# Kernel optimization log

Hardware: AMD Instinct MI355X
Metric: run time of the kernel (lower is better)

Reference implementation:

```python
import jax, jax.numpy as jnp
import numpy as np

N_NODES = 50000
N_EDGES = 640000
D = 128
BN_EPS = 1e-5
NEG_SLOPE = 0.2  # PyG GATv2Conv default negative_slope


def setup_inputs() -> dict:
    key = jax.random.key(0)
    ks = jax.random.split(key, 8)
    s = 1.0 / np.sqrt(D)
    x = jax.random.normal(ks[0], (N_NODES, D), dtype=jnp.float32)
    edge_index = jax.random.randint(ks[1], (2, N_EDGES), 0, N_NODES, dtype=jnp.int32)
    edge_attr = jax.random.uniform(ks[2], (N_EDGES, 1), dtype=jnp.float32)
    Wl = jax.random.normal(ks[3], (D, D), dtype=jnp.float32) * s
    Wr = jax.random.normal(ks[4], (D, D), dtype=jnp.float32) * s
    We = jax.random.normal(ks[5], (1, D), dtype=jnp.float32) * s
    att = jax.random.normal(ks[6], (D,), dtype=jnp.float32) * s
    return {
        "x": x, "edge_index": edge_index, "edge_attr": edge_attr,
        "Wl": Wl, "bl": jnp.zeros((D,), jnp.float32),
        "Wr": Wr, "br": jnp.zeros((D,), jnp.float32),
        "We": We, "att": att,
        "bias_out": jnp.zeros((D,), jnp.float32),
        "bn_gamma": jnp.ones((D,), jnp.float32),
        "bn_beta": jnp.zeros((D,), jnp.float32),
    }


def _gatv2(x, edge_index, edge_attr, Wl, bl, Wr, br, We, att, bias_out):
    # GATv2Conv, heads=1, concat=True, dropout treated as eval (p=0)
    src, dst = edge_index[0], edge_index[1]
    xl = x @ Wl + bl                      # source-side transform [N, D]
    xr = x @ Wr + br                      # target-side transform [N, D]
    e = edge_attr @ We                    # edge embedding       [E, D]
    m = xl[src] + xr[dst] + e             # gather + fuse        [E, D]
    m = jax.nn.leaky_relu(m, NEG_SLOPE)
    logits = m @ att                      # per-edge score [E]
    n = x.shape[0]
    # segment softmax over destination node neighborhoods
    mx = jax.ops.segment_max(logits, dst, num_segments=n)
    ex = jnp.exp(logits - mx[dst])
    den = jax.ops.segment_sum(ex, dst, num_segments=n)
    alpha = ex / (den[dst] + 1e-16)
    out = jax.ops.segment_sum(xl[src] * alpha[:, None], dst, num_segments=n)
    return out + bias_out


def reference(x, edge_index, edge_attr, Wl, bl, Wr, br, We, att, bias_out,
              bn_gamma, bn_beta):
    h = x + _gatv2(x, edge_index, edge_attr, Wl, bl, Wr, br, We, att, bias_out)
    h = jax.nn.gelu(h, approximate=False)  # torch nn.GELU default (erf)
    # BatchNorm over node dim, training-style batch stats (biased var)
    mean = jnp.mean(h, axis=0)
    var = jnp.mean((h - mean) ** 2, axis=0)
    h = (h - mean) * jax.lax.rsqrt(var + BN_EPS) * bn_gamma + bn_beta
    return h
```

## Files before the change

kernel.cpp:

```cpp
#include <hip/hip_runtime.h>
#include <math.h>

#define D 128
#define STATS_BLOCKS 512
#define SCAN_CHUNK 256

typedef __attribute__((ext_vector_type(8))) short short8;
typedef __attribute__((ext_vector_type(4))) float f32x4;

__device__ __forceinline__ unsigned short f2bf(float f) {
    unsigned u = __float_as_uint(f);
    unsigned r = (u + 0x7fff + ((u >> 16) & 1)) >> 16;
    return (unsigned short)r;
}

__global__ __launch_bounds__(256) void pack_w_k(const float* __restrict__ Wl,
    const float* __restrict__ Wr, unsigned short* __restrict__ wpack)
{
    const int lane = threadIdx.x & 63;
    const int wv = threadIdx.x >> 6;
    const int slot = blockIdx.x * 4 + wv;
    const int ct = slot >> 2;
    const int kt = slot & 3;
    const float* W = (ct < 8) ? Wl : Wr;
    const int cb = (ct & 7) * 16 + (lane & 15);
    const int kb = kt * 32 + (lane >> 4) * 8;
    unsigned short v[8];
#pragma unroll
    for (int i = 0; i < 8; i++) v[i] = f2bf(W[(size_t)(kb + i) * D + cb]);
    *(uint4*)(wpack + ((size_t)slot << 9) + lane * 8) = *(uint4*)v;
}

__global__ __launch_bounds__(256) void gemm_mfma_k(const float* __restrict__ x,
    const unsigned short* __restrict__ wpack, const float* __restrict__ bl,
    const float* __restrict__ br, unsigned* __restrict__ xlb,
    float* __restrict__ xr, int n)
{
    const int lane = threadIdx.x & 63;
    const int wv = threadIdx.x >> 6;
    const int rt = blockIdx.x * 4 + wv;
    if (rt * 16 >= n) return;
    const int r0 = rt * 16;
    const int ra = r0 + (lane & 15);
    const int r = ra < n ? ra : n - 1;
    const int ko = (lane >> 4) * 8;

    short8 a[4];
#pragma unroll
    for (int kt = 0; kt < 4; kt++) {
        const float* px = x + (size_t)r * D + kt * 32 + ko;
        float4 lo = *(const float4*)px;
        float4 hi = *(const float4*)(px + 4);
        short8 t;
        t[0] = (short)f2bf(lo.x); t[1] = (short)f2bf(lo.y);
        t[2] = (short)f2bf(lo.z); t[3] = (short)f2bf(lo.w);
        t[4] = (short)f2bf(hi.x); t[5] = (short)f2bf(hi.y);
        t[6] = (short)f2bf(hi.z); t[7] = (short)f2bf(hi.w);
        a[kt] = t;
    }

    f32x4 acc[16];
#pragma unroll
    for (int i = 0; i < 16; i++) acc[i] = (f32x4){0.f, 0.f, 0.f, 0.f};

#pragma unroll
    for (int kt = 0; kt < 4; kt++) {
#pragma unroll
        for (int ct = 0; ct < 16; ct++) {
            short8 b = *(const short8*)(wpack + (((size_t)(ct * 4 + kt)) << 9) + lane * 8);
            acc[ct] = __builtin_amdgcn_mfma_f32_16x16x32_bf16(a[kt], b, acc[ct], 0, 0, 0);
        }
    }

    const int colb = lane & 15;
    const int rbase = r0 + (lane >> 4) * 4;
#pragma unroll
    for (int ct = 8; ct < 16; ct++) {
        const int c = (ct - 8) * 16 + colb;
        const float bb = br[c];
#pragma unroll
        for (int reg = 0; reg < 4; reg++) {
            const int row = rbase + reg;
            if (row < n) xr[(size_t)row * D + c] = acc[ct][reg] + bb;
        }
    }
#pragma unroll
    for (int ct = 0; ct < 8; ct++) {
        const int c = ct * 16 + colb;
        const float bb = bl[c];
#pragma unroll
        for (int reg = 0; reg < 4; reg++) {
            unsigned mybf = f2bf(acc[ct][reg] + bb);
            unsigned other = (unsigned)__shfl_xor((int)mybf, 1);
            if ((lane & 1) == 0) {
                const int row = rbase + reg;
                if (row < n) xlb[(size_t)row * 64 + (c >> 1)] = mybf | (other << 16);
            }
        }
    }
}

__global__ __launch_bounds__(256) void hist_k(const int* __restrict__ ei,
    int* __restrict__ deg, int E)
{
    int e = blockIdx.x * blockDim.x + threadIdx.x;
    if (e < E) atomicAdd(&deg[ei[E + e]], 1);
}

__global__ __launch_bounds__(256) void scan_sum_k(const int* __restrict__ deg,
    int* __restrict__ bsum, int n)
{
    const int t = threadIdx.x;
    const int i = blockIdx.x * SCAN_CHUNK + t;
    int s = (i < n) ? deg[i] : 0;
#pragma unroll
    for (int off = 32; off > 0; off >>= 1) s += __shfl_xor(s, off);
    __shared__ int ws_[4];
    const int lane = t & 63, w = t >> 6;
    if (lane == 0) ws_[w] = s;
    __syncthreads();
    if (t == 0) bsum[blockIdx.x] = ws_[0] + ws_[1] + ws_[2] + ws_[3];
}

__global__ __launch_bounds__(256) void scan_off_k(const int* __restrict__ bsum,
    int* __restrict__ boff, int* __restrict__ rowptr, int nb, int n)
{
    const int t = threadIdx.x;
    int v = (t < nb) ? bsum[t] : 0;
    const int lane = t & 63, w = t >> 6;
    int inc = v;
#pragma unroll
    for (int off = 1; off < 64; off <<= 1) {
        int u = __shfl_up(inc, off);
        if (lane >= off) inc += u;
    }
    __shared__ int wsum[4], wpre[4];
    if (lane == 63) wsum[w] = inc;
    __syncthreads();
    if (t == 0) {
        int r = 0;
#pragma unroll
        for (int j = 0; j < 4; j++) { wpre[j] = r; r += wsum[j]; }
        rowptr[n] = r;
    }
    __syncthreads();
    if (t < nb) boff[t] = inc - v + wpre[w];
}

__global__ __launch_bounds__(256) void scan_fin_k(int* __restrict__ deg,
    const int* __restrict__ boff, int* __restrict__ rowptr, int n)
{
    const int t = threadIdx.x;
    const int i = blockIdx.x * SCAN_CHUNK + t;
    int v = (i < n) ? deg[i] : 0;
    const int lane = t & 63, w = t >> 6;
    int inc = v;
#pragma unroll
    for (int off = 1; off < 64; off <<= 1) {
        int u = __shfl_up(inc, off);
        if (lane >= off) inc += u;
    }
    __shared__ int wsum[4], wpre[4];
    if (lane == 63) wsum[w] = inc;
    __syncthreads();
    if (t == 0) {
        int r = 0;
#pragma unroll
        for (int j = 0; j < 4; j++) { wpre[j] = r; r += wsum[j]; }
    }
    __syncthreads();
    if (i < n) {
        int ex = inc - v + wpre[w] + boff[blockIdx.x];
        rowptr[i] = ex;
        deg[i] = ex;
    }
}

__global__ __launch_bounds__(256) void scatter_k(const int* __restrict__ ei,
    const float* __restrict__ ea, int* __restrict__ cursor,
    uint2* __restrict__ edges, int E)
{
    int e = blockIdx.x * blockDim.x + threadIdx.x;
    if (e >= E) return;
    int dst = ei[E + e];
    int pos = atomicAdd(&cursor[dst], 1);
    edges[pos] = make_uint2((unsigned)ei[e], __float_as_uint(ea[e]));
}

__global__ __launch_bounds__(256) void agg_k(const unsigned* __restrict__ xlb,
    const float* __restrict__ xr, const int* __restrict__ rowptr,
    const uint2* __restrict__ edges, const float* __restrict__ We,
    const float* __restrict__ att, float* __restrict__ out, int n)
{
    const int wave = threadIdx.x >> 6;
    const int lane = threadIdx.x & 63;
    const int g = lane >> 4;
    const int li = lane & 15;
    const int v = blockIdx.x * 4 + wave;
    if (v >= n) return;
    const int beg = rowptr[v];
    const int end = rowptr[v + 1];

    float xrv[8], wev[8], atv[8];
    {
        const int f0 = li * 8;
        float4 a0 = *(const float4*)(xr + (size_t)v * D + f0);
        float4 a1 = *(const float4*)(xr + (size_t)v * D + f0 + 4);
        xrv[0]=a0.x; xrv[1]=a0.y; xrv[2]=a0.z; xrv[3]=a0.w;
        xrv[4]=a1.x; xrv[5]=a1.y; xrv[6]=a1.z; xrv[7]=a1.w;
        float4 w0 = *(const float4*)(We + f0);
        float4 w1 = *(const float4*)(We + f0 + 4);
        wev[0]=w0.x; wev[1]=w0.y; wev[2]=w0.z; wev[3]=w0.w;
        wev[4]=w1.x; wev[5]=w1.y; wev[6]=w1.z; wev[7]=w1.w;
        float4 t0 = *(const float4*)(att + f0);
        float4 t1 = *(const float4*)(att + f0 + 4);
        atv[0]=t0.x; atv[1]=t0.y; atv[2]=t0.z; atv[3]=t0.w;
        atv[4]=t1.x; atv[5]=t1.y; atv[6]=t1.z; atv[7]=t1.w;
    }

    float m = -1e30f, s = 0.f;
    float acc[8];
#pragma unroll
    for (int k = 0; k < 8; k++) acc[k] = 0.f;

    int j = beg + g;
    uint2 e2 = make_uint2(0u, 0u);
    uint4 xb4 = make_uint4(0u, 0u, 0u, 0u);
    if (j < end) {
        e2 = edges[j];
        xb4 = *(const uint4*)(xlb + (size_t)e2.x * 64 + li * 4);
    }
    while (j < end) {
        const int jn = j + 4;
        const int jc = jn < end ? jn : end - 1;
        uint2 e2n = edges[jc];
        uint4 xbn = *(const uint4*)(xlb + (size_t)e2n.x * 64 + li * 4);

        const float eav = __uint_as_float(e2.y);
        float xv[8];
        xv[0] = __uint_as_float(xb4.x << 16); xv[1] = __uint_as_float(xb4.x & 0xffff0000u);
        xv[2] = __uint_as_float(xb4.y << 16); xv[3] = __uint_as_float(xb4.y & 0xffff0000u);
        xv[4] = __uint_as_float(xb4.z << 16); xv[5] = __uint_as_float(xb4.z & 0xffff0000u);
        xv[6] = __uint_as_float(xb4.w << 16); xv[7] = __uint_as_float(xb4.w & 0xffff0000u);

        float p = 0.f;
#pragma unroll
        for (int k = 0; k < 8; k++) {
            float t = fmaf(eav, wev[k], xrv[k]) + xv[k];
            t = fmaxf(t, 0.2f * t);
            p = fmaf(t, atv[k], p);
        }
#pragma unroll
        for (int off = 8; off >= 1; off >>= 1) p += __shfl_xor(p, off);

        const float pm = fmaxf(m, p);
        const float sc = __expf(m - pm);
        const float w  = __expf(p - pm);
        s = s * sc + w;
#pragma unroll
        for (int k = 0; k < 8; k++) acc[k] = fmaf(acc[k], sc, w * xv[k]);
        m = pm;

        e2 = e2n; xb4 = xbn; j = jn;
    }

#pragma unroll
    for (int off = 16; off <= 32; off <<= 1) {
        const float mo = __shfl_xor(m, off);
        const float so = __shfl_xor(s, off);
        const float pm = fmaxf(m, mo);
        const float sa = __expf(m - pm);
        const float sb = __expf(mo - pm);
        s = s * sa + so * sb;
#pragma unroll
        for (int k = 0; k < 8; k++)
            acc[k] = acc[k] * sa + __shfl_xor(acc[k], off) * sb;
        m = pm;
    }

    if (g == 0) {
        const float inv = 1.f / (s + 1e-16f);
        const int f0 = li * 8;
        float4 o0 = make_float4(acc[0]*inv, acc[1]*inv, acc[2]*inv, acc[3]*inv);
        float4 o1 = make_float4(acc[4]*inv, acc[5]*inv, acc[6]*inv, acc[7]*inv);
        *(float4*)(out + (size_t)v * D + f0) = o0;
        *(float4*)(out + (size_t)v * D + f0 + 4) = o1;
    }
}

__global__ __launch_bounds__(256) void gelu_stats_k(const float* __restrict__ x,
    const float* __restrict__ bias, float* __restrict__ h,
    float* __restrict__ partials, int total4)
{
    const int t = threadIdx.x;
    const int c0 = (t & 31) * 4;
    const float4 bv = *(const float4*)&bias[c0];
    float sum[4] = {0.f, 0.f, 0.f, 0.f}, sq[4] = {0.f, 0.f, 0.f, 0.f};
    const int stride = gridDim.x * blockDim.x;
    for (int i4 = blockIdx.x * blockDim.x + t; i4 < total4; i4 += stride) {
        float4 g4 = ((const float4*)h)[i4];
        float4 xv = ((const float4*)x)[i4];
        float hv[4] = {xv.x + g4.x + bv.x, xv.y + g4.y + bv.y,
                       xv.z + g4.z + bv.z, xv.w + g4.w + bv.w};
        float res[4];
#pragma unroll
        for (int j = 0; j < 4; j++) {
            float ge = 0.5f * hv[j] * (1.f + erff(hv[j] * 0.70710678118654752f));
            res[j] = ge;
            sum[j] += ge;
            sq[j] += ge * ge;
        }
        ((float4*)h)[i4] = make_float4(res[0], res[1], res[2], res[3]);
    }
    __shared__ float red[8][128];
    const int slot = t >> 5;
#pragma unroll
    for (int j = 0; j < 4; j++) red[slot][c0 + j] = sum[j];
    __syncthreads();
    if (t < 128) {
        float tot = 0.f;
#pragma unroll
        for (int s2 = 0; s2 < 8; s2++) tot += red[s2][t];
        partials[(size_t)t * STATS_BLOCKS + blockIdx.x] = tot;
    }
    __syncthreads();
#pragma unroll
    for (int j = 0; j < 4; j++) red[slot][c0 + j] = sq[j];
    __syncthreads();
    if (t < 128) {
        float tot = 0.f;
#pragma unroll
        for (int s2 = 0; s2 < 8; s2++) tot += red[s2][t];
        partials[(size_t)(128 + t) * STATS_BLOCKS + blockIdx.x] = tot;
    }
}

__global__ __launch_bounds__(256) void bn_reduce_params_k(const float* __restrict__ partials,
    const float* __restrict__ gamma, const float* __restrict__ beta,
    float* __restrict__ ab, float n)
{
    const int c = blockIdx.x;
    const int t = threadIdx.x;
    float s = 0.f, q = 0.f;
    for (int b = t; b < STATS_BLOCKS; b += 256) {
        s += partials[(size_t)c * STATS_BLOCKS + b];
        q += partials[(size_t)(128 + c) * STATS_BLOCKS + b];
    }
#pragma unroll
    for (int off = 32; off > 0; off >>= 1) {
        s += __shfl_xor(s, off);
        q += __shfl_xor(q, off);
    }
    __shared__ float ss[4], qq[4];
    const int lane = t & 63, w = t >> 6;
    if (lane == 0) { ss[w] = s; qq[w] = q; }
    __syncthreads();
    if (t == 0) {
        float S = ss[0] + ss[1] + ss[2] + ss[3];
        float Q = qq[0] + qq[1] + qq[2] + qq[3];
        float mean = S / n;
        float var = Q / n - mean * mean;
        float a = rsqrtf(var + 1e-5f) * gamma[c];
        ab[c] = a;
        ab[c + 128] = beta[c] - mean * a;
    }
}

__global__ __launch_bounds__(256) void bn_apply_k(float* __restrict__ h,
    const float* __restrict__ ab, int total4)
{
    int i4 = blockIdx.x * blockDim.x + threadIdx.x;
    if (i4 >= total4) return;
    int cg = i4 & 31;
    float4 v = ((const float4*)h)[i4];
    float4 a = ((const float4*)ab)[cg];
    float4 b = ((const float4*)(ab + 128))[cg];
    ((float4*)h)[i4] = make_float4(v.x * a.x + b.x, v.y * a.y + b.y,
                                   v.z * a.z + b.z, v.w * a.w + b.w);
}

extern "C" void kernel_launch(void* const* d_in, const int* in_sizes, int n_in,
                              void* d_out, int out_size, void* d_ws, size_t ws_size,
                              hipStream_t stream)
{
    const float* x    = (const float*)d_in[0];
    const int*   ei   = (const int*)d_in[1];
    const float* ea   = (const float*)d_in[2];
    const float* Wl   = (const float*)d_in[3];
    const float* bl   = (const float*)d_in[4];
    const float* Wr   = (const float*)d_in[5];
    const float* br   = (const float*)d_in[6];
    const float* We   = (const float*)d_in[7];
    const float* att  = (const float*)d_in[8];
    const float* bias = (const float*)d_in[9];
    const float* gamma= (const float*)d_in[10];
    const float* beta = (const float*)d_in[11];
    float* out = (float*)d_out;

    const int n = in_sizes[0] / D;
    const int E = in_sizes[1] / 2;
    const int nb = (n + SCAN_CHUNK - 1) / SCAN_CHUNK;

    char* ws = (char*)d_ws;
    unsigned short* wpack = (unsigned short*)ws;
    unsigned* xlb = (unsigned*)(ws + 65536);
    float* xr = (float*)(xlb + (size_t)n * 64);
    int* deg = (int*)(xr + (size_t)n * D);
    int* rowptr = deg + n;
    uintptr_t ep = ((uintptr_t)(rowptr + n + 1) + 7) & ~(uintptr_t)7;
    uint2* edges = (uint2*)ep;
    float* partials = (float*)(edges + E);
    int* bsum = (int*)(partials + 256 * STATS_BLOCKS);
    int* boff = bsum + nb;
    float* ab = (float*)(boff + nb);

    hipMemsetAsync(deg, 0, (size_t)n * 4, stream);

    pack_w_k<<<16, 256, 0, stream>>>(Wl, Wr, wpack);
    const int nrt = (n + 15) / 16;
    gemm_mfma_k<<<(nrt + 3) / 4, 256, 0, stream>>>(x, wpack, bl, br, xlb, xr, n);
    hist_k<<<(E + 255) / 256, 256, 0, stream>>>(ei, deg, E);
    scan_sum_k<<<nb, 256, 0, stream>>>(deg, bsum, n);
    scan_off_k<<<1, 256, 0, stream>>>(bsum, boff, rowptr, nb, n);
    scan_fin_k<<<nb, 256, 0, stream>>>(deg, boff, rowptr, n);
    scatter_k<<<(E + 255) / 256, 256, 0, stream>>>(ei, ea, deg, edges, E);
    agg_k<<<(n + 3) / 4, 256, 0, stream>>>(xlb, xr, rowptr, edges, We, att, out, n);
    const int total4 = (n * D) / 4;
    gelu_stats_k<<<STATS_BLOCKS, 256, 0, stream>>>(x, bias, out, partials, total4);
    bn_reduce_params_k<<<128, 256, 0, stream>>>(partials, gamma, beta, ab, (float)n);
    bn_apply_k<<<(total4 + 255) / 256, 256, 0, stream>>>(out, ab, total4);
}
```

Baseline: 173.7 us.

## Degree-sort nodes, assign one 16-lane group per node, store intermediates in bf16

Builds a degree histogram inside the scan kernels and counting-sorts nodes by in-degree into a node order array. The aggregation kernel then gives each 16-lane group one node, so neighbouring groups in a wave have similar edge counts, and the cross-group softmax merge is removed. The aggregation output and the GELU result are stored as bf16 to cut memory traffic in the elementwise passes, and the xlb buffer is reused to hold the GELU result. This trades extra precision loss and some scan-kernel work for better load balance and less bandwidth.

```diff
diff --git a/kernel.cpp b/kernel.cpp
--- a/kernel.cpp
+++ b/kernel.cpp
@@ -13,6 +13,8 @@
     unsigned r = (u + 0x7fff + ((u >> 16) & 1)) >> 16;
     return (unsigned short)r;
 }
+__device__ __forceinline__ float bflo(unsigned u) { return __uint_as_float(u << 16); }
+__device__ __forceinline__ float bfhi(unsigned u) { return __uint_as_float(u & 0xffff0000u); }
 
 __global__ __launch_bounds__(256) void pack_w_k(const float* __restrict__ Wl,
     const float* __restrict__ Wr, unsigned short* __restrict__ wpack)
@@ -108,11 +110,18 @@
 }
 
 __global__ __launch_bounds__(256) void scan_sum_k(const int* __restrict__ deg,
-    int* __restrict__ bsum, int n)
-{
+    int* __restrict__ bsum, int* __restrict__ deghist, int n)
+{
+    __shared__ int lh[256];
     const int t = threadIdx.x;
+    lh[t] = 0;
+    __syncthreads();
     const int i = blockIdx.x * SCAN_CHUNK + t;
-    int s = (i < n) ? deg[i] : 0;
+    int s = 0;
+    if (i < n) {
+        s = deg[i];
+        atomicAdd(&lh[min(s, 255)], 1);
+    }
 #pragma unroll
     for (int off = 32; off > 0; off >>= 1) s += __shfl_xor(s, off);
     __shared__ int ws_[4];
@@ -120,14 +129,16 @@
     if (lane == 0) ws_[w] = s;
     __syncthreads();
     if (t == 0) bsum[blockIdx.x] = ws_[0] + ws_[1] + ws_[2] + ws_[3];
+    if (lh[t]) atomicAdd(&deghist[t], lh[t]);
 }
 
 __global__ __launch_bounds__(256) void scan_off_k(const int* __restrict__ bsum,
-    int* __restrict__ boff, int* __restrict__ rowptr, int nb, int n)
+    int* __restrict__ boff, int* __restrict__ rowptr,
+    const int* __restrict__ deghist, int* __restrict__ degcur, int nb, int n)
 {
     const int t = threadIdx.x;
+    const int lane = t & 63, w = t >> 6;
     int v = (t < nb) ? bsum[t] : 0;
-    const int lane = t & 63, w = t >> 6;
     int inc = v;
 #pragma unroll
     for (int off = 1; off < 64; off <<= 1) {
@@ -145,14 +156,36 @@
     }
     __syncthreads();
     if (t < nb) boff[t] = inc - v + wpre[w];
+    int dv = deghist[t];
+    int dinc = dv;
+#pragma unroll
+    for (int off = 1; off < 64; off <<= 1) {
+        int u = __shfl_up(dinc, off);
+        if (lane >= off) dinc += u;
+    }
+    __shared__ int w2sum[4], w2pre[4];
+    if (lane == 63) w2sum[w] = dinc;
+    __syncthreads();
+    if (t == 0) {
+        int r = 0;
+#pragma unroll
+        for (int j = 0; j < 4; j++) { w2pre[j] = r; r += w2sum[j]; }
+    }
+    __syncthreads();
+    degcur[t] = dinc - dv + w2pre[w];
 }
 
 __global__ __launch_bounds__(256) void scan_fin_k(int* __restrict__ deg,
-    const int* __restrict__ boff, int* __restrict__ rowptr, int n)
-{
+    const int* __restrict__ boff, int* __restrict__ rowptr,
+    int* __restrict__ degcur, int* __restrict__ nodeord, int n)
+{
+    __shared__ int wsum[4], wpre[4];
+    __shared__ int lh[256], lbase[256];
     const int t = threadIdx.x;
     const int i = blockIdx.x * SCAN_CHUNK + t;
+    lh[t] = 0;
     int v = (i < n) ? deg[i] : 0;
+    const int bin = min(v, 255);
     const int lane = t & 63, w = t >> 6;
     int inc = v;
 #pragma unroll
@@ -160,7 +193,6 @@
         int u = __shfl_up(inc, off);
         if (lane >= off) inc += u;
     }
-    __shared__ int wsum[4], wpre[4];
     if (lane == 63) wsum[w] = inc;
     __syncthreads();
     if (t == 0) {
@@ -169,11 +201,17 @@
         for (int j = 0; j < 4; j++) { wpre[j] = r; r += wsum[j]; }
     }
     __syncthreads();
+    int rank = 0;
     if (i < n) {
+        rank = atomicAdd(&lh[bin], 1);
         int ex = inc - v + wpre[w] + boff[blockIdx.x];
         rowptr[i] = ex;
         deg[i] = ex;
     }
+    __syncthreads();
+    lbase[t] = lh[t] ? atomicAdd(&degcur[t], lh[t]) : 0;
+    __syncthreads();
+    if (i < n) nodeord[lbase[bin] + rank] = i;
 }
 
 __global__ __launch_bounds__(256) void scatter_k(const int* __restrict__ ei,
@@ -190,20 +228,19 @@
 __global__ __launch_bounds__(256) void agg_k(const unsigned* __restrict__ xlb,
     const float* __restrict__ xr, const int* __restrict__ rowptr,
     const uint2* __restrict__ edges, const float* __restrict__ We,
-    const float* __restrict__ att, float* __restrict__ out, int n)
-{
-    const int wave = threadIdx.x >> 6;
-    const int lane = threadIdx.x & 63;
-    const int g = lane >> 4;
-    const int li = lane & 15;
-    const int v = blockIdx.x * 4 + wave;
-    if (v >= n) return;
+    const float* __restrict__ att, const int* __restrict__ nodeord,
+    unsigned* __restrict__ aggout, int n)
+{
+    const int gg = (blockIdx.x * 256 + threadIdx.x) >> 4;
+    const int li = threadIdx.x & 15;
+    if (gg >= n) return;
+    const int v = nodeord[gg];
     const int beg = rowptr[v];
     const int end = rowptr[v + 1];
+    const int f0 = li * 8;
 
     float xrv[8], wev[8], atv[8];
     {
-        const int f0 = li * 8;
         float4 a0 = *(const float4*)(xr + (size_t)v * D + f0);
         float4 a1 = *(const float4*)(xr + (size_t)v * D + f0 + 4);
         xrv[0]=a0.x; xrv[1]=a0.y; xrv[2]=a0.z; xrv[3]=a0.w;
@@ -223,7 +260,7 @@
 #pragma unroll
     for (int k = 0; k < 8; k++) acc[k] = 0.f;
 
-    int j = beg + g;
+    int j = beg;
     uint2 e2 = make_uint2(0u, 0u);
     uint4 xb4 = make_uint4(0u, 0u, 0u, 0u);
     if (j < end) {
@@ -231,17 +268,17 @@
         xb4 = *(const uint4*)(xlb + (size_t)e2.x * 64 + li * 4);
     }
     while (j < end) {
-        const int jn = j + 4;
+        const int jn = j + 1;
         const int jc = jn < end ? jn : end - 1;
-        uint2 e2n = edges[jc];
-        uint4 xbn = *(const uint4*)(xlb + (size_t)e2n.x * 64 + li * 4);
+        const uint2 e2n = edges[jc];
+        const uint4 xbn = *(const uint4*)(xlb + (size_t)e2n.x * 64 + li * 4);
 
         const float eav = __uint_as_float(e2.y);
         float xv[8];
-        xv[0] = __uint_as_float(xb4.x << 16); xv[1] = __uint_as_float(xb4.x & 0xffff0000u);
-        xv[2] = __uint_as_float(xb4.y << 16); xv[3] = __uint_as_float(xb4.y & 0xffff0000u);
-        xv[4] = __uint_as_float(xb4.z << 16); xv[5] = __uint_as_float(xb4.z & 0xffff0000u);
-        xv[6] = __uint_as_float(xb4.w << 16); xv[7] = __uint_as_float(xb4.w & 0xffff0000u);
+        xv[0] = bflo(xb4.x); xv[1] = bfhi(xb4.x);
+        xv[2] = bflo(xb4.y); xv[3] = bfhi(xb4.y);
+        xv[4] = bflo(xb4.z); xv[5] = bfhi(xb4.z);
+        xv[6] = bflo(xb4.w); xv[7] = bfhi(xb4.w);
 
         float p = 0.f;
 #pragma unroll
@@ -264,33 +301,17 @@
         e2 = e2n; xb4 = xbn; j = jn;
     }
 
-#pragma unroll
-    for (int off = 16; off <= 32; off <<= 1) {
-        const float mo = __shfl_xor(m, off);
-        const float so = __shfl_xor(s, off);
-        const float pm = fmaxf(m, mo);
-        const float sa = __expf(m - pm);
-        const float sb = __expf(mo - pm);
-        s = s * sa + so * sb;
-#pragma unroll
-        for (int k = 0; k < 8; k++)
-            acc[k] = acc[k] * sa + __shfl_xor(acc[k], off) * sb;
-        m = pm;
-    }
-
-    if (g == 0) {
-        const float inv = 1.f / (s + 1e-16f);
-        const int f0 = li * 8;
-        float4 o0 = make_float4(acc[0]*inv, acc[1]*inv, acc[2]*inv, acc[3]*inv);
-        float4 o1 = make_float4(acc[4]*inv, acc[5]*inv, acc[6]*inv, acc[7]*inv);
-        *(float4*)(out + (size_t)v * D + f0) = o0;
-        *(float4*)(out + (size_t)v * D + f0 + 4) = o1;
-    }
+    const float inv = 1.f / (s + 1e-16f);
+    unsigned o0 = (unsigned)f2bf(acc[0]*inv) | ((unsigned)f2bf(acc[1]*inv) << 16);
+    unsigned o1 = (unsigned)f2bf(acc[2]*inv) | ((unsigned)f2bf(acc[3]*inv) << 16);
+    unsigned o2 = (unsigned)f2bf(acc[4]*inv) | ((unsigned)f2bf(acc[5]*inv) << 16);
+    unsigned o3 = (unsigned)f2bf(acc[6]*inv) | ((unsigned)f2bf(acc[7]*inv) << 16);
+    *(uint4*)(aggout + (size_t)v * 64 + li * 4) = make_uint4(o0, o1, o2, o3);
 }
 
 __global__ __launch_bounds__(256) void gelu_stats_k(const float* __restrict__ x,
-    const float* __restrict__ bias, float* __restrict__ h,
-    float* __restrict__ partials, int total4)
+    const float* __restrict__ bias, const unsigned* __restrict__ aggout,
+    unsigned* __restrict__ hbf, float* __restrict__ partials, int total4)
 {
     const int t = threadIdx.x;
     const int c0 = (t & 31) * 4;
@@ -298,10 +319,10 @@
     float sum[4] = {0.f, 0.f, 0.f, 0.f}, sq[4] = {0.f, 0.f, 0.f, 0.f};
     const int stride = gridDim.x * blockDim.x;
     for (int i4 = blockIdx.x * blockDim.x + t; i4 < total4; i4 += stride) {
-        float4 g4 = ((const float4*)h)[i4];
         float4 xv = ((const float4*)x)[i4];
-        float hv[4] = {xv.x + g4.x + bv.x, xv.y + g4.y + bv.y,
-                       xv.z + g4.z + bv.z, xv.w + g4.w + bv.w};
+        uint2 ag = *(const uint2*)(aggout + (size_t)i4 * 2);
+        float hv[4] = {xv.x + bflo(ag.x) + bv.x, xv.y + bfhi(ag.x) + bv.y,
+                       xv.z + bflo(ag.y) + bv.z, xv.w + bfhi(ag.y) + bv.w};
         float res[4];
 #pragma unroll
         for (int j = 0; j < 4; j++) {
@@ -310,7 +331,10 @@
             sum[j] += ge;
             sq[j] += ge * ge;
         }
-        ((float4*)h)[i4] = make_float4(res[0], res[1], res[2], res[3]);
+        uint2 hp;
+        hp.x = (unsigned)f2bf(res[0]) | ((unsigned)f2bf(res[1]) << 16);
+        hp.y = (unsigned)f2bf(res[2]) | ((unsigned)f2bf(res[3]) << 16);
+        *(uint2*)(hbf + (size_t)i4 * 2) = hp;
     }
     __shared__ float red[8][128];
     const int slot = t >> 5;
@@ -366,17 +390,17 @@
     }
 }
 
-__global__ __launch_bounds__(256) void bn_apply_k(float* __restrict__ h,
-    const float* __restrict__ ab, int total4)
+__global__ __launch_bounds__(256) void bn_apply_k(const unsigned* __restrict__ hbf,
+    float* __restrict__ out, const float* __restrict__ ab, int total4)
 {
     int i4 = blockIdx.x * blockDim.x + threadIdx.x;
     if (i4 >= total4) return;
     int cg = i4 & 31;
-    float4 v = ((const float4*)h)[i4];
+    uint2 hp = *(const uint2*)(hbf + (size_t)i4 * 2);
     float4 a = ((const float4*)ab)[cg];
     float4 b = ((const float4*)(ab + 128))[cg];
-    ((float4*)h)[i4] = make_float4(v.x * a.x + b.x, v.y * a.y + b.y,
-                                   v.z * a.z + b.z, v.w * a.w + b.w);
+    ((float4*)out)[i4] = make_float4(bflo(hp.x) * a.x + b.x, bfhi(hp.x) * a.y + b.y,
+                                     bflo(hp.y) * a.z + b.z, bfhi(hp.y) * a.w + b.w);
 }
 
 extern "C" void kernel_launch(void* const* d_in, const int* in_sizes, int n_in,
@@ -407,26 +431,32 @@
     float* xr = (float*)(xlb + (size_t)n * 64);
     int* deg = (int*)(xr + (size_t)n * D);
     int* rowptr = deg + n;
-    uintptr_t ep = ((uintptr_t)(rowptr + n + 1) + 7) & ~(uintptr_t)7;
+    int* deghist = rowptr + n + 1;
+    int* degcur = deghist + 256;
+    int* nodeord = degcur + 256;
+    int* bsum = nodeord + n;
+    int* boff = bsum + nb;
+    uintptr_t ep = ((uintptr_t)(boff + nb) + 7) & ~(uintptr_t)7;
     uint2* edges = (uint2*)ep;
     float* partials = (float*)(edges + E);
-    int* bsum = (int*)(partials + 256 * STATS_BLOCKS);
-    int* boff = bsum + nb;
-    float* ab = (float*)(boff + nb);
-
-    hipMemsetAsync(deg, 0, (size_t)n * 4, stream);
+    float* ab = partials + 256 * STATS_BLOCKS;
+
+    unsigned* aggout = (unsigned*)d_out;
+    unsigned* hbf = xlb;
+
+    hipMemsetAsync(deg, 0, (size_t)(2 * n + 1 + 256) * 4, stream);
 
     pack_w_k<<<16, 256, 0, stream>>>(Wl, Wr, wpack);
     const int nrt = (n + 15) / 16;
     gemm_mfma_k<<<(nrt + 3) / 4, 256, 0, stream>>>(x, wpack, bl, br, xlb, xr, n);
     hist_k<<<(E + 255) / 256, 256, 0, stream>>>(ei, deg, E);
-    scan_sum_k<<<nb, 256, 0, stream>>>(deg, bsum, n);
-    scan_off_k<<<1, 256, 0, stream>>>(bsum, boff, rowptr, nb, n);
-    scan_fin_k<<<nb, 256, 0, stream>>>(deg, boff, rowptr, n);
+    scan_sum_k<<<nb, 256, 0, stream>>>(deg, bsum, deghist, n);
+    scan_off_k<<<1, 256, 0, stream>>>(bsum, boff, rowptr, deghist, degcur, nb, n);
+    scan_fin_k<<<nb, 256, 0, stream>>>(deg, boff, rowptr, degcur, nodeord, n);
     scatter_k<<<(E + 255) / 256, 256, 0, stream>>>(ei, ea, deg, edges, E);
-    agg_k<<<(n + 3) / 4, 256, 0, stream>>>(xlb, xr, rowptr, edges, We, att, out, n);
+    agg_k<<<(n + 15) / 16, 256, 0, stream>>>(xlb, xr, rowptr, edges, We, att, nodeord, aggout, n);
     const int total4 = (n * D) / 4;
-    gelu_stats_k<<<STATS_BLOCKS, 256, 0, stream>>>(x, bias, out, partials, total4);
+    gelu_stats_k<<<STATS_BLOCKS, 256, 0, stream>>>(x, bias, aggout, hbf, partials, total4);
     bn_reduce_params_k<<<128, 256, 0, stream>>>(partials, gamma, beta, ab, (float)n);
-    bn_apply_k<<<(total4 + 255) / 256, 256, 0, stream>>>(out, ab, total4);
-}
+    bn_apply_k<<<(total4 + 255) / 256, 256, 0, stream>>>(hbf, out, ab, total4);
+}
```

New measurement: 181.8 us. 4.6% more time.
